# Optimization experiments

Hardware: AMD Instinct MI355X
Metric: run time of the kernel (lower is better)

The kernel has to match this reference:

```python
import jax, jax.numpy as jnp
import numpy as np

B, S, D, H = 2, 2048, 1024, 16
A = D // H
NEG = -1e9


def setup_inputs() -> dict:
    key = jax.random.key(0)
    ks = jax.random.split(key, 5)
    std = 1.0 / np.sqrt(D)
    query = jax.random.normal(ks[0], (B, S, D), dtype=jnp.float32)
    context = jax.random.normal(ks[1], (B, S, D), dtype=jnp.float32)
    Wq = jax.random.normal(ks[2], (D, D), dtype=jnp.float32) * std
    Wkv = jax.random.normal(ks[3], (2 * D, D), dtype=jnp.float32) * std
    Wout = jax.random.normal(ks[4], (D, D), dtype=jnp.float32) * std
    # 2D additive causal mask [q_len, c_len]; module broadcasts it over batch and heads
    mask = jnp.where(jnp.tril(jnp.ones((S, S), dtype=bool)), 0.0, NEG).astype(jnp.float32)
    return {"query": query, "context": context, "Wq": Wq, "Wkv": Wkv, "Wout": Wout, "mask": mask}


def reference(query, context, Wq, Wkv, Wout, mask):
    b, q_len, d = query.shape
    c_len = context.shape[1]
    h, a = H, A
    scale = 1.0 / np.sqrt(d)  # NOTE: module scales by 1/sqrt(hidden_dim), not head dim

    q = query @ Wq.T                      # [b, q, d]
    kv = context @ Wkv.T                  # [b, c, 2d]
    k, v = jnp.split(kv, 2, axis=-1)

    q = q.reshape(b, q_len, h, a)
    k = k.reshape(b, c_len, h, a)
    v = v.reshape(b, c_len, h, a)

    scores = jnp.einsum('bqha,bkha->bqkh', q, k)      # [b, q, k, h]
    scores = scores + mask[None, :, :, None]          # mask added BEFORE scaling (faithful)
    attn = jax.nn.softmax(scores * scale, axis=2)     # softmax over key dim
    out = jnp.einsum('bqkh,bkha->bqha', attn, v).reshape(b, q_len, d)
    return out @ Wout.T
```

## Files before the change

### kernel.cpp

```cpp
#include <hip/hip_runtime.h>
#include <hip/hip_bf16.h>
#include <stdint.h>

#define S_LEN 2048
#define DIM   1024
#define NH    16
#define HD    64
#define BATCH 2

typedef __attribute__((ext_vector_type(4))) float f32x4;
typedef __attribute__((ext_vector_type(16))) float f32x16;
typedef __attribute__((ext_vector_type(8))) short bf16x8;
typedef __attribute__((ext_vector_type(4))) int i32x4;
typedef __hip_bfloat16 bf16;

__device__ inline void gload_lds16(const void* g, void* l) {
  __builtin_amdgcn_global_load_lds(
      (const __attribute__((address_space(1))) void*)g,
      (__attribute__((address_space(3))) void*)l, 16, 0, 0);
}

__device__ inline bf16x8 as_bf16x8(i32x4 x) {
  union { i32x4 i; bf16x8 v; } u; u.i = x; return u.v;
}
__device__ inline int cvt_pk_bf16(float lo, float hi) {
  int r;
  asm("v_cvt_pk_bf16_f32 %0, %1, %2" : "=v"(r) : "v"(lo), "v"(hi));
  return r;
}
__device__ inline float b2f(short s) {
  union { unsigned int u; float f; } w;
  w.u = ((unsigned int)(unsigned short)s) << 16;
  return w.f;
}

__global__ __launch_bounds__(256) void cvt_all(
    const float* __restrict__ q, const float* __restrict__ c,
    const float* __restrict__ wq, const float* __restrict__ wkv,
    const float* __restrict__ wo,
    bf16* __restrict__ oq, bf16* __restrict__ oc, bf16* __restrict__ owq,
    bf16* __restrict__ owkv, bf16* __restrict__ owo) {
  const int N0 = 1048576, N1 = 1048576, N2 = 262144, N3 = 524288, N4 = 262144;
  const int total = N0 + N1 + N2 + N3 + N4;
  for (int i = blockIdx.x * 256 + threadIdx.x; i < total; i += gridDim.x * 256) {
    const float* src; bf16* dst; int off = i;
    if (i < N0)                { src = q;   dst = oq; }
    else if (i < N0 + N1)      { src = c;   dst = oc;   off -= N0; }
    else if (i < N0 + N1 + N2) { src = wq;  dst = owq;  off -= N0 + N1; }
    else if (i < N0 + N1 + N2 + N3) { src = wkv; dst = owkv; off -= N0 + N1 + N2; }
    else                       { src = wo;  dst = owo;  off -= N0 + N1 + N2 + N3; }
    float4 v = ((const float4*)src)[off];
    bf16 b0 = __float2bfloat16(v.x), b1 = __float2bfloat16(v.y);
    bf16 b2 = __float2bfloat16(v.z), b3 = __float2bfloat16(v.w);
    ushort4 o;
    o.x = *(unsigned short*)&b0; o.y = *(unsigned short*)&b1;
    o.z = *(unsigned short*)&b2; o.w = *(unsigned short*)&b3;
    ((ushort4*)dst)[off] = o;
  }
}

__device__ inline void gemm128_body(const bf16* __restrict__ A, const bf16* __restrict__ B,
                                    bf16* __restrict__ C, int N, int K, float alpha,
                                    int bm, int bn, bf16* Als, bf16* Bls) {
  const int tid = threadIdx.x;
  const int lane = tid & 63, wid = tid >> 6;
  const int wr = wid >> 1, wc = wid & 1;
  const int fr = lane & 15, fq = lane >> 4;

  f32x4 acc[4][4] = {};
  const int kTiles = K >> 5;
  for (int kt = 0; kt < kTiles; ++kt) {
    const int k0 = kt << 5;
    __syncthreads();
#pragma unroll
    for (int j = 0; j < 2; ++j) {
      int ob = wid * 2048 + j * 1024;
      int o = ob + lane * 16;
      int r = o >> 6;
      int kk = (o & 63) >> 1;
      gload_lds16(A + (size_t)(bm + r) * K + k0 + kk, (char*)Als + ob);
      gload_lds16(B + (size_t)(bn + r) * K + k0 + kk, (char*)Bls + ob);
    }
    __syncthreads();
    bf16x8 af[4], bfr[4];
#pragma unroll
    for (int m = 0; m < 4; ++m)
      af[m] = *(const bf16x8*)(Als + (wr * 64 + m * 16 + fr) * 32 + fq * 8);
#pragma unroll
    for (int n = 0; n < 4; ++n)
      bfr[n] = *(const bf16x8*)(Bls + (wc * 64 + n * 16 + fr) * 32 + fq * 8);
#pragma unroll
    for (int m = 0; m < 4; ++m)
#pragma unroll
      for (int n = 0; n < 4; ++n)
        acc[m][n] = __builtin_amdgcn_mfma_f32_16x16x32_bf16(af[m], bfr[n], acc[m][n], 0, 0, 0);
  }
#pragma unroll
  for (int m = 0; m < 4; ++m)
#pragma unroll
    for (int n = 0; n < 4; ++n)
#pragma unroll
      for (int i = 0; i < 4; ++i) {
        int row = bm + wr * 64 + m * 16 + fq * 4 + i;
        int col = bn + wc * 64 + n * 16 + fr;
        C[(size_t)row * N + col] = __float2bfloat16(acc[m][n][i] * alpha);
      }
}

__global__ __launch_bounds__(256) void gemm_proj(
    const bf16* __restrict__ Aq, const bf16* __restrict__ Bq, bf16* __restrict__ Cq,
    const bf16* __restrict__ Akv, const bf16* __restrict__ Bkv, bf16* __restrict__ Ckv,
    float qalpha) {
  __shared__ __align__(16) bf16 Als[128 * 32];
  __shared__ __align__(16) bf16 Bls[128 * 32];
  const int bid = blockIdx.x;
  const bf16 *A, *B; bf16 *C; int N; float alpha; int bx, by;
  if (bid < 256) { A = Aq;  B = Bq;  C = Cq;  N = 1024; alpha = qalpha; bx = bid & 7;  by = bid >> 3; }
  else { int t = bid - 256; A = Akv; B = Bkv; C = Ckv; N = 2048; alpha = 1.0f; bx = t & 15; by = t >> 4; }
  gemm128_body(A, B, C, N, 1024, alpha, by * 128, bx * 128, Als, Bls);
}

__global__ __launch_bounds__(256) void gemm_bt_n64(
    const bf16* __restrict__ A, const bf16* __restrict__ B,
    float* __restrict__ C, int M, int N, int K) {
  __shared__ __align__(16) bf16 Als[128 * 32];
  __shared__ __align__(16) bf16 Bls[64 * 32];
  const int tid = threadIdx.x;
  const int lane = tid & 63, wid = tid >> 6;
  const int bm = blockIdx.y * 128, bn = blockIdx.x * 64;
  const int fr = lane & 15, fq = lane >> 4;

  f32x4 acc[2][4] = {};
  const int kTiles = K >> 5;
  for (int kt = 0; kt < kTiles; ++kt) {
    const int k0 = kt << 5;
    __syncthreads();
#pragma unroll
    for (int j = 0; j < 2; ++j) {
      int ob = wid * 2048 + j * 1024;
      int o = ob + lane * 16;
      int r = o >> 6;
      int kk = (o & 63) >> 1;
      gload_lds16(A + (size_t)(bm + r) * K + k0 + kk, (char*)Als + ob);
    }
    {
      int ob = wid * 1024;
      int o = ob + lane * 16;
      int r = o >> 6;
      int kk = (o & 63) >> 1;
      gload_lds16(B + (size_t)(bn + r) * K + k0 + kk, (char*)Bls + ob);
    }
    __syncthreads();
    bf16x8 af[2], bfr[4];
#pragma unroll
    for (int m = 0; m < 2; ++m)
      af[m] = *(const bf16x8*)(Als + (wid * 32 + m * 16 + fr) * 32 + fq * 8);
#pragma unroll
    for (int n = 0; n < 4; ++n)
      bfr[n] = *(const bf16x8*)(Bls + (n * 16 + fr) * 32 + fq * 8);
#pragma unroll
    for (int m = 0; m < 2; ++m)
#pragma unroll
      for (int n = 0; n < 4; ++n)
        acc[m][n] = __builtin_amdgcn_mfma_f32_16x16x32_bf16(af[m], bfr[n], acc[m][n], 0, 0, 0);
  }
#pragma unroll
  for (int m = 0; m < 2; ++m)
#pragma unroll
    for (int n = 0; n < 4; ++n)
#pragma unroll
      for (int i = 0; i < 4; ++i) {
        int row = bm + wid * 32 + m * 16 + fq * 4 + i;
        int col = bn + n * 16 + fr;
        C[(size_t)row * N + col] = acc[m][n][i];
      }
}

__global__ __launch_bounds__(256) void transpose_v(
    const bf16* __restrict__ KV, bf16* __restrict__ Vt) {
  __shared__ __align__(16) bf16 tile[64][72];
  const int t = threadIdx.x;
  const int s0 = blockIdx.x * 64, h = blockIdx.y, b = blockIdx.z;
#pragma unroll
  for (int j = 0; j < 2; ++j) {
    int s = j * 32 + (t >> 3);
    int a = (t & 7) * 8;
    bf16x8 v = *(const bf16x8*)(KV + (size_t)(b * S_LEN + s0 + s) * (2 * DIM) + DIM + h * HD + a);
    *(bf16x8*)&tile[s][a] = v;
  }
  __syncthreads();
#pragma unroll
  for (int j = 0; j < 2; ++j) {
    int a = j * 32 + (t >> 3);
    int sc = (t & 7) * 8;
    bf16x8 v;
#pragma unroll
    for (int e = 0; e < 8; ++e)
      ((short*)&v)[e] = *(const short*)&tile[sc + e][a];
    *(bf16x8*)(Vt + (size_t)((b * NH + h) * HD + a) * S_LEN + s0 + sc) = v;
  }
}

__global__ __launch_bounds__(256, 4) void attn_fwd(
    const bf16* __restrict__ Q,
    const bf16* __restrict__ KV,
    const bf16* __restrict__ Vt,
    bf16* __restrict__ Opart,
    float* __restrict__ Rpart) {
  __shared__ __align__(16) bf16 Kls[3][64 * 64];
  __shared__ __align__(16) bf16 Vls[3][64 * 64];
  const int tid = threadIdx.x, lane = tid & 63, wid = tid >> 6;
  const int l31 = lane & 31, hi = lane >> 5;
  const int bid = blockIdx.x;
  const int qx = 15 - (bid >> 6);
  const int rem = bid & 63;
  const int c = rem >> 5;
  const int hb = rem & 31;
  const int h = hb >> 1, b = hb & 1;
  const int rw0 = qx * 128 + wid * 32;
  const int qrow = rw0 + l31;
  const float NEGINF = -__builtin_inff();

  const int cnt = qx + 1;
  const int kt0 = c * cnt;
  const int p = ((b * NH + h) * 32) + qx * 2 + c;

  bf16x8 qf[4];
#pragma unroll
  for (int ka = 0; ka < 4; ++ka)
    qf[ka] = *(const bf16x8*)(Q + (size_t)(b * S_LEN + qrow) * DIM + h * HD + ka * 16 + hi * 8);

  f32x16 oacc[2] = {};
  float rsA[4] = {0.f, 0.f, 0.f, 0.f};

  auto stage = [&](int buf, int kt) {
#pragma unroll
    for (int j = 0; j < 2; ++j) {
      int ob = (wid * 2 + j) * 1024;
      int o = ob + lane * 16;
      int r = o >> 7;
      int sb = (o & 127) ^ ((r & 7) << 4);
      gload_lds16(KV + (size_t)(b * S_LEN + kt * 64 + r) * (2 * DIM) + h * HD + (sb >> 1),
                  (char*)Kls[buf] + ob);
      gload_lds16(Vt + (size_t)((b * NH + h) * HD + r) * S_LEN + kt * 64 + (sb >> 1),
                  (char*)Vls[buf] + ob);
    }
  };

  stage(0, kt0);
  if (cnt > 1) stage(1, kt0 + 1);

  for (int i = 0; i < cnt; ++i) {
    const int kt = kt0 + i;
    if (i + 1 < cnt) asm volatile("s_waitcnt vmcnt(4)" ::: "memory");
    else             asm volatile("s_waitcnt vmcnt(0)" ::: "memory");
    __syncthreads();

    const int cb = i % 3;
    if (64 * kt <= rw0 + 31) {
      const bf16* Kb = Kls[cb];
      const bf16* Vb = Vls[cb];
      const bool maskt = (64 * kt + 63 > rw0);

#pragma unroll
      for (int kb = 0; kb < 2; ++kb) {
        f32x16 cc = {};
        __builtin_amdgcn_s_setprio(1);
#pragma unroll
        for (int ka = 0; ka < 4; ++ka) {
          int row = kb * 32 + l31;
          bf16x8 kf = *(const bf16x8*)((const char*)Kb + row * 128 +
                                       ((ka * 32 + hi * 16) ^ ((row & 7) << 4)));
          cc = __builtin_amdgcn_mfma_f32_32x32x16_bf16(kf, qf[ka], cc, 0, 0, 0);
        }
        __builtin_amdgcn_s_setprio(0);

        float pe[16];
        if (maskt) {
#pragma unroll
          for (int r = 0; r < 16; ++r) {
            int key = kt * 64 + kb * 32 + (r & 3) + 8 * (r >> 2) + 4 * hi;
            float s = (key <= qrow) ? cc[r] : NEGINF;
            pe[r] = __builtin_amdgcn_exp2f(s);
            rsA[r & 3] += pe[r];
          }
        } else {
#pragma unroll
          for (int r = 0; r < 16; ++r) {
            pe[r] = __builtin_amdgcn_exp2f(cc[r]);
            rsA[r & 3] += pe[r];
          }
        }

        int u[8], x[8];
#pragma unroll
        for (int t = 0; t < 8; ++t) u[t] = cvt_pk_bf16(pe[2 * t], pe[2 * t + 1]);
#pragma unroll
        for (int t = 0; t < 8; ++t) x[t] = __shfl_xor(u[t], 32);
        i32x4 w0, w1;
        w0[0] = hi ? x[2] : u[0]; w0[1] = hi ? x[3] : u[1];
        w0[2] = hi ? u[2] : x[0]; w0[3] = hi ? u[3] : x[1];
        w1[0] = hi ? x[6] : u[4]; w1[1] = hi ? x[7] : u[5];
        w1[2] = hi ? u[6] : x[4]; w1[3] = hi ? u[7] : x[5];
        bf16x8 pa0 = as_bf16x8(w0), pa1 = as_bf16x8(w1);

        __builtin_amdgcn_s_setprio(1);
#pragma unroll
        for (int pl = 0; pl < 2; ++pl) {
          bf16x8 pa = pl ? pa1 : pa0;
#pragma unroll
          for (int nb = 0; nb < 2; ++nb) {
            int a = nb * 32 + l31;
            bf16x8 vf = *(const bf16x8*)((const char*)Vb + a * 128 +
                                         ((kb * 64 + pl * 32 + hi * 16) ^ ((a & 7) << 4)));
            oacc[nb] = __builtin_amdgcn_mfma_f32_32x32x16_bf16(pa, vf, oacc[nb], 0, 0, 0);
          }
        }
        __builtin_amdgcn_s_setprio(0);
      }
    }

    if (i + 2 < cnt) stage((i + 2) % 3, kt0 + i + 2);
  }

  float rsum = (rsA[0] + rsA[1]) + (rsA[2] + rsA[3]);
  rsum += __shfl_xor(rsum, 32);
  if (hi == 0) Rpart[p * 128 + wid * 32 + l31] = rsum;
#pragma unroll
  for (int nb = 0; nb < 2; ++nb)
#pragma unroll
    for (int r = 0; r < 16; ++r) {
      int qloc = (r & 3) + 8 * (r >> 2) + 4 * hi;
      Opart[(size_t)p * 8192 + (wid * 32 + qloc) * 64 + nb * 32 + l31] =
          __float2bfloat16(oacc[nb][r]);
    }
}

__global__ __launch_bounds__(256) void attn_combine(
    const bf16* __restrict__ Opart, const float* __restrict__ Rpart,
    bf16* __restrict__ O) {
  const int g = blockIdx.x;
  const int qx = g & 15, bh = g >> 4;
  const int h = bh & 15, b = bh >> 4;
  const int t = threadIdx.x;
  const int row = t >> 1, col0 = (t & 1) * 32;
  const int p0 = bh * 32 + qx * 2;
  const size_t o0 = (size_t)p0 * 8192 + row * 64 + col0;
  const float rinv = 1.0f / (Rpart[p0 * 128 + row] + Rpart[p0 * 128 + 128 + row]);
  const int s = qx * 128 + row;
  bf16* dst = O + (size_t)(b * S_LEN + s) * DIM + h * HD + col0;
#pragma unroll
  for (int j = 0; j < 4; ++j) {
    bf16x8 a = *(const bf16x8*)(Opart + o0 + j * 8);
    bf16x8 cc = *(const bf16x8*)(Opart + o0 + 8192 + j * 8);
    bf16x8 w;
#pragma unroll
    for (int e = 0; e < 8; ++e) {
      bf16 r = __float2bfloat16((b2f(a[e]) + b2f(cc[e])) * rinv);
      ((short*)&w)[e] = *(short*)&r;
    }
    *(bf16x8*)(dst + j * 8) = w;
  }
}

extern "C" void kernel_launch(void* const* d_in, const int* in_sizes, int n_in,
                              void* d_out, int out_size, void* d_ws, size_t ws_size,
                              hipStream_t stream) {
  (void)in_sizes; (void)n_in; (void)out_size; (void)ws_size;
  const float* query   = (const float*)d_in[0];
  const float* context = (const float*)d_in[1];
  const float* Wq      = (const float*)d_in[2];
  const float* Wkv     = (const float*)d_in[3];
  const float* Wout    = (const float*)d_in[4];
  float* out = (float*)d_out;

  bf16* ws = (bf16*)d_ws;
  const size_t nBSD = (size_t)BATCH * S_LEN * DIM;
  bf16* qbf    = ws;
  bf16* cbf    = qbf + nBSD;
  bf16* wqbf   = cbf + nBSD;
  bf16* wkvbf  = wqbf + (size_t)DIM * DIM;
  bf16* woutbf = wkvbf + (size_t)2 * DIM * DIM;
  bf16* Qp     = woutbf + (size_t)DIM * DIM;
  bf16* KVp    = Qp + nBSD;
  bf16* Vtp    = KVp + 2 * nBSD;
  bf16* Op     = Vtp + nBSD;
  bf16*  Opart = qbf;
  float* Rpart = (float*)wqbf;

  cvt_all<<<2048, 256, 0, stream>>>(query, context, Wq, Wkv, Wout,
                                    qbf, cbf, wqbf, wkvbf, woutbf);

  gemm_proj<<<768, 256, 0, stream>>>(qbf, wqbf, Qp, cbf, wkvbf, KVp, 0.0450842200277801f);

  transpose_v<<<dim3(S_LEN / 64, NH, BATCH), 256, 0, stream>>>(KVp, Vtp);
  attn_fwd<<<1024, 256, 0, stream>>>(Qp, KVp, Vtp, Opart, Rpart);
  attn_combine<<<512, 256, 0, stream>>>(Opart, Rpart, Op);
  const int M = BATCH * S_LEN;
  gemm_bt_n64<<<dim3(DIM / 64, M / 128), 256, 0, stream>>>(Op, woutbf, out, M, DIM, DIM);
}
```

Baseline: 120.4 us.

## Fuse V transpose into projection GEMM epilogue and use permlane32 swap in attention

```diff
diff --git a/kernel.cpp b/kernel.cpp
--- a/kernel.cpp
+++ b/kernel.cpp
@@ -59,9 +59,20 @@
   }
 }
 
-__device__ inline void gemm128_body(const bf16* __restrict__ A, const bf16* __restrict__ B,
-                                    bf16* __restrict__ C, int N, int K, float alpha,
-                                    int bm, int bn, bf16* Als, bf16* Bls) {
+__global__ __launch_bounds__(256) void gemm_proj(
+    const bf16* __restrict__ Aq, const bf16* __restrict__ Bq, bf16* __restrict__ Cq,
+    const bf16* __restrict__ Akv, const bf16* __restrict__ Bkv, bf16* __restrict__ Ckv,
+    bf16* __restrict__ Vt, float qalpha) {
+  __shared__ __align__(16) bf16 Als[128 * 32];
+  __shared__ __align__(16) bf16 Bls[128 * 32];
+  const int bid = blockIdx.x;
+  const bf16 *A, *B; bf16 *C; int N; float alpha; int bx, by;
+  if (bid < 256) { A = Aq;  B = Bq;  C = Cq;  N = 1024; alpha = qalpha; bx = bid & 7;  by = bid >> 3; }
+  else { int t = bid - 256; A = Akv; B = Bkv; C = Ckv; N = 2048; alpha = 1.0f; bx = t & 15; by = t >> 4; }
+  const bool vtmode = (bid >= 256) && (bx >= 8);
+  const int bm = by * 128, bn = bx * 128;
+  const int K = 1024;
+
   const int tid = threadIdx.x;
   const int lane = tid & 63, wid = tid >> 6;
   const int wr = wid >> 1, wc = wid & 1;
@@ -95,29 +106,34 @@
       for (int n = 0; n < 4; ++n)
         acc[m][n] = __builtin_amdgcn_mfma_f32_16x16x32_bf16(af[m], bfr[n], acc[m][n], 0, 0, 0);
   }
-#pragma unroll
-  for (int m = 0; m < 4; ++m)
-#pragma unroll
-    for (int n = 0; n < 4; ++n)
-#pragma unroll
-      for (int i = 0; i < 4; ++i) {
-        int row = bm + wr * 64 + m * 16 + fq * 4 + i;
-        int col = bn + wc * 64 + n * 16 + fr;
-        C[(size_t)row * N + col] = __float2bfloat16(acc[m][n][i] * alpha);
+
+  if (!vtmode) {
+#pragma unroll
+    for (int m = 0; m < 4; ++m)
+#pragma unroll
+      for (int n = 0; n < 4; ++n)
+#pragma unroll
+        for (int i = 0; i < 4; ++i) {
+          int row = bm + wr * 64 + m * 16 + fq * 4 + i;
+          int col = bn + wc * 64 + n * 16 + fr;
+          C[(size_t)row * N + col] = __float2bfloat16(acc[m][n][i] * alpha);
+        }
+  } else {
+#pragma unroll
+    for (int m = 0; m < 4; ++m) {
+      int row0 = bm + wr * 64 + m * 16 + fq * 4;
+      int b = row0 >> 11, s0 = row0 & 2047;
+#pragma unroll
+      for (int n = 0; n < 4; ++n) {
+        int ag = bn + wc * 64 + n * 16 + fr - 1024;
+        int h = ag >> 6, a = ag & 63;
+        uint2 pk;
+        pk.x = (unsigned)cvt_pk_bf16(acc[m][n][0], acc[m][n][1]);
+        pk.y = (unsigned)cvt_pk_bf16(acc[m][n][2], acc[m][n][3]);
+        *(uint2*)(Vt + (size_t)((b * NH + h) * HD + a) * S_LEN + s0) = pk;
       }
-}
-
-__global__ __launch_bounds__(256) void gemm_proj(
-    const bf16* __restrict__ Aq, const bf16* __restrict__ Bq, bf16* __restrict__ Cq,
-    const bf16* __restrict__ Akv, const bf16* __restrict__ Bkv, bf16* __restrict__ Ckv,
-    float qalpha) {
-  __shared__ __align__(16) bf16 Als[128 * 32];
-  __shared__ __align__(16) bf16 Bls[128 * 32];
-  const int bid = blockIdx.x;
-  const bf16 *A, *B; bf16 *C; int N; float alpha; int bx, by;
-  if (bid < 256) { A = Aq;  B = Bq;  C = Cq;  N = 1024; alpha = qalpha; bx = bid & 7;  by = bid >> 3; }
-  else { int t = bid - 256; A = Akv; B = Bkv; C = Ckv; N = 2048; alpha = 1.0f; bx = t & 15; by = t >> 4; }
-  gemm128_body(A, B, C, N, 1024, alpha, by * 128, bx * 128, Als, Bls);
+    }
+  }
 }
 
 __global__ __launch_bounds__(256) void gemm_bt_n64(
@@ -174,31 +190,6 @@
         int col = bn + n * 16 + fr;
         C[(size_t)row * N + col] = acc[m][n][i];
       }
-}
-
-__global__ __launch_bounds__(256) void transpose_v(
-    const bf16* __restrict__ KV, bf16* __restrict__ Vt) {
-  __shared__ __align__(16) bf16 tile[64][72];
-  const int t = threadIdx.x;
-  const int s0 = blockIdx.x * 64, h = blockIdx.y, b = blockIdx.z;
-#pragma unroll
-  for (int j = 0; j < 2; ++j) {
-    int s = j * 32 + (t >> 3);
-    int a = (t & 7) * 8;
-    bf16x8 v = *(const bf16x8*)(KV + (size_t)(b * S_LEN + s0 + s) * (2 * DIM) + DIM + h * HD + a);
-    *(bf16x8*)&tile[s][a] = v;
-  }
-  __syncthreads();
-#pragma unroll
-  for (int j = 0; j < 2; ++j) {
-    int a = j * 32 + (t >> 3);
-    int sc = (t & 7) * 8;
-    bf16x8 v;
-#pragma unroll
-    for (int e = 0; e < 8; ++e)
-      ((short*)&v)[e] = *(const short*)&tile[sc + e][a];
-    *(bf16x8*)(Vt + (size_t)((b * NH + h) * HD + a) * S_LEN + s0 + sc) = v;
-  }
 }
 
 __global__ __launch_bounds__(256, 4) void attn_fwd(
@@ -254,7 +245,8 @@
     const int kt = kt0 + i;
     if (i + 1 < cnt) asm volatile("s_waitcnt vmcnt(4)" ::: "memory");
     else             asm volatile("s_waitcnt vmcnt(0)" ::: "memory");
-    __syncthreads();
+    __builtin_amdgcn_s_barrier();
+    __builtin_amdgcn_sched_barrier(0);
 
     const int cb = i % 3;
     if (64 * kt <= rw0 + 31) {
@@ -292,16 +284,17 @@
           }
         }
 
-        int u[8], x[8];
-#pragma unroll
-        for (int t = 0; t < 8; ++t) u[t] = cvt_pk_bf16(pe[2 * t], pe[2 * t + 1]);
-#pragma unroll
-        for (int t = 0; t < 8; ++t) x[t] = __shfl_xor(u[t], 32);
+        int u0 = cvt_pk_bf16(pe[0], pe[1]),  u1 = cvt_pk_bf16(pe[2], pe[3]);
+        int u2 = cvt_pk_bf16(pe[4], pe[5]),  u3 = cvt_pk_bf16(pe[6], pe[7]);
+        int u4 = cvt_pk_bf16(pe[8], pe[9]),  u5 = cvt_pk_bf16(pe[10], pe[11]);
+        int u6 = cvt_pk_bf16(pe[12], pe[13]), u7 = cvt_pk_bf16(pe[14], pe[15]);
+        asm("v_permlane32_swap_b32 %0, %1" : "+v"(u0), "+v"(u2));
+        asm("v_permlane32_swap_b32 %0, %1" : "+v"(u1), "+v"(u3));
+        asm("v_permlane32_swap_b32 %0, %1" : "+v"(u4), "+v"(u6));
+        asm("v_permlane32_swap_b32 %0, %1" : "+v"(u5), "+v"(u7));
         i32x4 w0, w1;
-        w0[0] = hi ? x[2] : u[0]; w0[1] = hi ? x[3] : u[1];
-        w0[2] = hi ? u[2] : x[0]; w0[3] = hi ? u[3] : x[1];
-        w1[0] = hi ? x[6] : u[4]; w1[1] = hi ? x[7] : u[5];
-        w1[2] = hi ? u[6] : x[4]; w1[3] = hi ? u[7] : x[5];
+        w0[0] = u0; w0[1] = u1; w0[2] = u2; w0[3] = u3;
+        w1[0] = u4; w1[1] = u5; w1[2] = u6; w1[3] = u7;
         bf16x8 pa0 = as_bf16x8(w0), pa1 = as_bf16x8(w1);
 
         __builtin_amdgcn_s_setprio(1);
@@ -391,9 +384,9 @@
   cvt_all<<<2048, 256, 0, stream>>>(query, context, Wq, Wkv, Wout,
                                     qbf, cbf, wqbf, wkvbf, woutbf);
 
-  gemm_proj<<<768, 256, 0, stream>>>(qbf, wqbf, Qp, cbf, wkvbf, KVp, 0.0450842200277801f);
-
-  transpose_v<<<dim3(S_LEN / 64, NH, BATCH), 256, 0, stream>>>(KVp, Vtp);
+  gemm_proj<<<768, 256, 0, stream>>>(qbf, wqbf, Qp, cbf, wkvbf, KVp, Vtp,
+                                     0.0450842200277801f);
+
   attn_fwd<<<1024, 256, 0, stream>>>(Qp, KVp, Vtp, Opart, Rpart);
   attn_combine<<<512, 256, 0, stream>>>(Opart, Rpart, Op);
   const int M = BATCH * S_LEN;
```

Result: slower. 129.4 us (+7.5%).
